# Kernel tuning notes

Measured on AMD Instinct MI355X. Metric: run time of the kernel, lower is better.

The kernel has to match this reference:

```python
import jax, jax.numpy as jnp
import numpy as np

THRESHOLD = 1.0
BETA = 0.9  # initial mem is zeros, so mem = beta*0 + u = u


def spike(u):
    # forward of SurrogateGradient: (u > threshold).float()
    return (u > THRESHOLD).astype(u.dtype)


def rope_tables(seq_len, head_dim, base=10000.0):
    inv_freq = 1.0 / (base ** (jnp.arange(0, head_dim, 2, dtype=jnp.float32) / head_dim))
    t = jnp.arange(seq_len, dtype=jnp.float32)
    freqs = jnp.einsum('i,j->ij', t, inv_freq)          # [S, d/2]
    emb = jnp.concatenate([freqs, freqs], axis=-1)       # [S, d]
    return jnp.cos(emb), jnp.sin(emb)


def apply_rope(x, cos, sin):
    # x: [B, S, H, d]
    x1, x2 = jnp.split(x, 2, axis=-1)
    rot = jnp.concatenate([-x2, x1], axis=-1)
    return x * cos[None, :, None, :] + rot * sin[None, :, None, :]


def setup_inputs() -> dict:
    key = jax.random.key(0)
    ks = jax.random.split(key, 5)
    B, S, D = 1, 2048, 2048
    std = 1.0 / np.sqrt(D)
    return {
        'x':  jax.random.normal(ks[0], (B, S, D), jnp.float32),
        'Wq': jax.random.normal(ks[1], (D, D), jnp.float32) * std,
        'Wk': jax.random.normal(ks[2], (D, D), jnp.float32) * std,
        'Wv': jax.random.normal(ks[3], (D, D), jnp.float32) * std,
        'Wo': jax.random.normal(ks[4], (D, D), jnp.float32) * std,
    }


def reference(x, Wq, Wk, Wv, Wo):
    B, S, D = x.shape
    H, hd = 16, 128
    scale = hd ** -0.5

    q = (x @ Wq).reshape(B, S, H, hd)
    k = (x @ Wk).reshape(B, S, H, hd)
    v = (x @ Wv).reshape(B, S, H, hd)

    # LIF: mem starts at zero -> mem = q; spike = (mem > threshold)
    sq, sk, sv = spike(q), spike(k), spike(v)

    cos, sin = rope_tables(S, hd)
    rq = apply_rope(sq, cos, sin)
    rk = apply_rope(sk, cos, sin)

    scores = jnp.einsum('bqhd,bkhd->bhqk', rq, rk) * scale  # [B,H,S,S]
    causal = jnp.tril(jnp.ones((S, S), dtype=bool))
    scores = jnp.where(causal[None, None], scores, -jnp.inf)
    attn = jax.nn.softmax(scores, axis=-1)

    out = jnp.einsum('bhqk,bkhd->bqhd', attn, sv).reshape(B, S, H * hd)
    return out @ Wo
```

## Files before the change

### kernel.cpp

```cpp
#include <hip/hip_runtime.h>

typedef unsigned short u16;
typedef unsigned int u32;
typedef u16 u16x4 __attribute__((ext_vector_type(4)));
typedef u16 u16x8 __attribute__((ext_vector_type(8)));
typedef float f32x4 __attribute__((ext_vector_type(4)));
typedef __bf16 bf16x8 __attribute__((ext_vector_type(8)));
typedef _Float16 f16x4 __attribute__((ext_vector_type(4)));
typedef _Float16 f16x8 __attribute__((ext_vector_type(8)));

#define DD 2048
#define SCALE_ATTN 0.08838834764831845f
#define DELTA 0.005f

#define GL16(g, l)                                                              \
  __builtin_amdgcn_global_load_lds((const __attribute__((address_space(1))) u32*)(g), \
                                   (__attribute__((address_space(3))) u32*)(l), 16, 0, 0)

__device__ __forceinline__ u16 f2bf(float f) {
  u32 u = __float_as_uint(f);
  u32 r = (u + 0x7FFFu + ((u >> 16) & 1u)) >> 16;
  return (u16)r;
}
__device__ __forceinline__ float bf2f(u16 h) { return __uint_as_float(((u32)h) << 16); }


__global__ void k_rope_tables(float* __restrict__ cosT, float* __restrict__ sinT) {
  int i = blockIdx.x * 256 + threadIdx.x;
  int s = i >> 6, j = i & 63;
  float e = (float)(2 * j) / 128.0f;
  float inv = 1.0f / powf(10000.0f, e);
  float fr = (float)s * inv;
  cosT[i] = cosf(fr);
  sinT[i] = sinf(fr);
}

__global__ void k_cvt_x(const float* __restrict__ x, _Float16* __restrict__ xf) {
  int i = (blockIdx.x * 256 + threadIdx.x) * 4;
  float4 v = *(const float4*)&x[i];
  f16x4 o = {(_Float16)v.x, (_Float16)v.y, (_Float16)v.z, (_Float16)v.w};
  *(f16x4*)&xf[i] = o;
}

__global__ void k_transpose_w(const float* __restrict__ Wq, const float* __restrict__ Wk,
                              const float* __restrict__ Wv, _Float16* __restrict__ Wq16,
                              _Float16* __restrict__ Wk16, _Float16* __restrict__ Wv16,
                              float* __restrict__ Wq32, float* __restrict__ Wk32,
                              float* __restrict__ Wv32) {
  const float* W = blockIdx.y == 0 ? Wq : (blockIdx.y == 1 ? Wk : Wv);
  _Float16* WT16 = blockIdx.y == 0 ? Wq16 : (blockIdx.y == 1 ? Wk16 : Wv16);
  float* WT32 = blockIdx.y == 0 ? Wq32 : (blockIdx.y == 1 ? Wk32 : Wv32);
  __shared__ float tile[32][33];
  int bk = blockIdx.x & 63, bn = blockIdx.x >> 6;
  int c = threadIdx.x & 31, r0 = threadIdx.x >> 5;
#pragma unroll
  for (int i = 0; i < 4; ++i) {
    int r = r0 + i * 8;
    tile[r][c] = W[(size_t)(bk * 32 + r) * DD + bn * 32 + c];
  }
  __syncthreads();
#pragma unroll
  for (int i = 0; i < 4; ++i) {
    int r = r0 + i * 8;
    float v = tile[c][r];
    size_t o = (size_t)(bn * 32 + r) * DD + bk * 32 + c;
    WT16[o] = (_Float16)v;
    WT32[o] = v;
  }
}

__global__ void k_transpose_bo(const float* __restrict__ W, u16* __restrict__ WhT) {
  __shared__ float tile[32][33];
  int bk = blockIdx.x & 63, bn = blockIdx.x >> 6;
  int c = threadIdx.x & 31, r0 = threadIdx.x >> 5;
#pragma unroll
  for (int i = 0; i < 4; ++i) {
    int r = r0 + i * 8;
    tile[r][c] = W[(size_t)(bk * 32 + r) * DD + bn * 32 + c];
  }
  __syncthreads();
#pragma unroll
  for (int i = 0; i < 4; ++i) {
    int r = r0 + i * 8;
    WhT[(size_t)(bn * 32 + r) * DD + bk * 32 + c] = f2bf(tile[c][r]);
  }
}

__global__ void k_transpose_bf16(const u16* __restrict__ in, u16* __restrict__ out) {
  __shared__ u16 tile[32][33];
  int bk = blockIdx.x & 63, bn = blockIdx.x >> 6;
  int c = threadIdx.x & 31, r0 = threadIdx.x >> 5;
#pragma unroll
  for (int i = 0; i < 4; ++i) {
    int r = r0 + i * 8;
    tile[r][c] = in[(size_t)(bk * 32 + r) * DD + bn * 32 + c];
  }
  __syncthreads();
#pragma unroll
  for (int i = 0; i < 4; ++i) {
    int r = r0 + i * 8;
    out[(size_t)(bn * 32 + r) * DD + bk * 32 + c] = tile[c][r];
  }
}

__global__ void k_rope_apply(u16* sq, u16* sk, const float* __restrict__ cosT,
                             const float* __restrict__ sinT) {
  int i = blockIdx.x * 256 + threadIdx.x;
  int s = i >> 10;
  int rest = i & 1023;
  int h = rest >> 6, j = rest & 63;
  size_t base = (size_t)s * DD + h * 128 + j;
  float c = cosT[(s << 6) | j], sn = sinT[(s << 6) | j];
  float a = bf2f(sq[base]), b = bf2f(sq[base + 64]);
  sq[base] = f2bf(a * c - b * sn);
  sq[base + 64] = f2bf(b * c + a * sn);
  a = bf2f(sk[base]);
  b = bf2f(sk[base + 64]);
  sk[base] = f2bf(a * c - b * sn);
  sk[base + 64] = f2bf(b * c + a * sn);
}

__global__ __launch_bounds__(256) void k_gemm_qkv(
    const _Float16* __restrict__ xf, const _Float16* __restrict__ BqT,
    const _Float16* __restrict__ BkT, const _Float16* __restrict__ BvT, u16* __restrict__ Sq,
    u16* __restrict__ Sk, u16* __restrict__ Sv, unsigned char* __restrict__ flagT) {
  __shared__ u16 lA[2 * 4096];
  __shared__ u16 lB[2 * 4096];

  const _Float16* BT = blockIdx.y == 0 ? BqT : (blockIdx.y == 1 ? BkT : BvT);
  u16* Out = blockIdx.y == 0 ? Sq : (blockIdx.y == 1 ? Sk : Sv);
  unsigned char* flT = flagT + (size_t)blockIdx.y * 4194304;

  int bid = blockIdx.x;
  int swz = (bid & 7) * 32 + (bid >> 3);
  int m0 = (swz >> 4) * 128, n0 = (swz & 15) * 128;

  int tid = threadIdx.x;
  int lane = tid & 63;
  int w = tid >> 6;
  int wr = (w >> 1) * 64, wc = (w & 1) * 64;
  int l15 = lane & 15, g8 = (lane >> 4) * 8;

  int ar0 = tid >> 2, ac0 = (tid & 3) << 3;
  int ar1 = (tid + 256) >> 2, ac1 = (tid & 3) << 3;

  f32x4 zero = {0.f, 0.f, 0.f, 0.f};
  f32x4 acc[4][4];
#pragma unroll
  for (int i = 0; i < 4; ++i)
#pragma unroll
    for (int j = 0; j < 4; ++j) acc[i][j] = zero;

  u16* laBase0 = lA + w * 512;
  u16* laBase1 = lA + 2048 + w * 512;
  u16* lbBase0 = lB + w * 512;
  u16* lbBase1 = lB + 2048 + w * 512;

  auto stage = [&](int buf, int vs) {
    int k0 = vs << 5;
    int bo = buf * 4096;
    GL16(&xf[(size_t)(m0 + ar0) * DD + k0 + ac0], laBase0 + bo);
    GL16(&xf[(size_t)(m0 + ar1) * DD + k0 + ac1], laBase1 + bo);
    GL16(&BT[(size_t)(n0 + ar0) * DD + k0 + ac0], lbBase0 + bo);
    GL16(&BT[(size_t)(n0 + ar1) * DD + k0 + ac1], lbBase1 + bo);
  };

  stage(0, 0);
  __syncthreads();
  for (int vs = 0; vs < 64; ++vs) {
    int cur = vs & 1;
    if (vs + 1 < 64) stage(cur ^ 1, vs + 1);
    const u16* la = lA + cur * 4096;
    const u16* lb = lB + cur * 4096;
    f16x8 af[4], bfr[4];
#pragma unroll
    for (int i = 0; i < 4; ++i) af[i] = *(const f16x8*)&la[(wr + i * 16 + l15) * 32 + g8];
#pragma unroll
    for (int j = 0; j < 4; ++j) bfr[j] = *(const f16x8*)&lb[(wc + j * 16 + l15) * 32 + g8];
#pragma unroll
    for (int i = 0; i < 4; ++i)
#pragma unroll
      for (int j = 0; j < 4; ++j)
        acc[i][j] = __builtin_amdgcn_mfma_f32_16x16x32_f16(af[i], bfr[j], acc[i][j], 0, 0, 0);
    __syncthreads();
  }

  int g4 = (lane >> 4) * 4;
#pragma unroll
  for (int i = 0; i < 4; ++i) {
    int row0 = m0 + wr + i * 16 + g4;
#pragma unroll
    for (int j = 0; j < 4; ++j) {
      int col = n0 + wc + j * 16 + l15;
      u32 fw = 0;
#pragma unroll
      for (int r = 0; r < 4; ++r) {
        float u = acc[i][j][r];
        Out[(size_t)(row0 + r) * DD + col] = (u > 1.0f) ? (u16)0x3F80 : (u16)0;
        if (fabsf(u - 1.0f) < DELTA) fw |= (1u << (8 * r));
      }
      *(u32*)&flT[(size_t)col * 2048 + row0] = fw;
    }
  }
}

__global__ __launch_bounds__(256) void k_compact(const unsigned char* __restrict__ flagT,
                                                 u32* __restrict__ cnt, u32* __restrict__ wlist) {
  __shared__ u32 wsum[4];
  int tid = threadIdx.x;
  int lane = tid & 63;
  int w = tid >> 6;
  size_t blockBase = (size_t)blockIdx.x * 16384;
  const u32* fp = (const u32*)(flagT + blockBase);
  unsigned long long fm = 0;
#pragma unroll
  for (int it = 0; it < 4; ++it) {
    u32 m16 = 0;
#pragma unroll
    for (int wd = 0; wd < 4; ++wd) {
      u32 v = fp[it * 1024 + tid * 4 + wd];
      m16 |= (((v >> 0) & 1u) | ((v >> 7) & 2u) | ((v >> 14) & 4u) | ((v >> 21) & 8u)) << (wd * 4);
    }
    fm |= (unsigned long long)m16 << (it * 16);
  }
  u32 c = (u32)__popcll(fm);
  u32 pre = c;
#pragma unroll
  for (int d = 1; d < 64; d <<= 1) {
    u32 t = __shfl_up(pre, d, 64);
    if (lane >= d) pre += t;
  }
  if (lane == 63) wsum[w] = pre;
  __syncthreads();
  u32 wbase = 0;
#pragma unroll
  for (int i = 0; i < 4; ++i)
    if (i < w) wbase += wsum[i];
  if (tid == 0) {
    u32 tot = wsum[0] + wsum[1] + wsum[2] + wsum[3];
    cnt[blockIdx.x] = tot > 256u ? 256u : tot;
  }
  u32 pos = wbase + pre - c;
  u32 outbase = (u32)blockIdx.x * 256u;
  while (fm) {
    int p = __ffsll((long long)fm) - 1;
    fm &= fm - 1;
    u32 e = (u32)blockBase + (u32)(p >> 4) * 4096u + (u32)tid * 16u + (u32)(p & 15);
    if (pos < 256u) wlist[outbase + pos] = e;
    ++pos;
  }
}

__global__ __launch_bounds__(256) void k_fixup(
    const float* __restrict__ x, const float* __restrict__ WqT, const float* __restrict__ WkT,
    const float* __restrict__ WvT, const u32* __restrict__ cnt, const u32* __restrict__ wlist,
    u16* __restrict__ Sq, u16* __restrict__ Sk, u16* __restrict__ Sv) {
  u32 wid = (blockIdx.x * 256 + threadIdx.x) >> 6;
  int lane = threadIdx.x & 63;
  for (u32 s = wid; s < 768u * 256u; s += 8192u) {
    u32 b = s % 768u, k = s / 768u;
    if (k >= cnt[b]) continue;
    u32 e = wlist[b * 256u + k];
    int i = (int)(e & 2047u);
    int j = (int)((e >> 11) & 2047u);
    int mat = (int)(e >> 22);
    const float* WT = mat == 0 ? WqT : (mat == 1 ? WkT : WvT);
    const float* xr = x + (size_t)i * DD;
    const float* wrw = WT + (size_t)j * DD;
    float u = 0.f;
#pragma unroll
    for (int t = 0; t < 8; ++t) {
      float4 a = *(const float4*)&xr[t * 256 + lane * 4];
      float4 bv = *(const float4*)&wrw[t * 256 + lane * 4];
      u = fmaf(a.x, bv.x, u);
      u = fmaf(a.y, bv.y, u);
      u = fmaf(a.z, bv.z, u);
      u = fmaf(a.w, bv.w, u);
    }
#pragma unroll
    for (int sh = 32; sh; sh >>= 1) u += __shfl_xor(u, sh);
    if (lane == 0) {
      u16* Out2 = mat == 0 ? Sq : (mat == 1 ? Sk : Sv);
      Out2[(size_t)i * DD + j] = (u > 1.0f) ? (u16)0x3F80 : (u16)0;
    }
  }
}

__global__ __launch_bounds__(256) void k_gemm_out(const u16* __restrict__ A,
                                                  const u16* __restrict__ BT,
                                                  float* __restrict__ C) {
  __shared__ u16 lA[2 * 4096];
  __shared__ u16 lB[2 * 4096];
  int bid = blockIdx.x;
  int swz = (bid & 7) * 32 + (bid >> 3);
  int m0 = (swz >> 4) * 128, n0 = (swz & 15) * 128;
  int tid = threadIdx.x;
  int lane = tid & 63;
  int w = tid >> 6;
  int wr = (w >> 1) * 64, wc = (w & 1) * 64;
  int l15 = lane & 15, g8 = (lane >> 4) * 8;
  int ar0 = tid >> 2, ac0 = (tid & 3) << 3;
  int ar1 = (tid + 256) >> 2, ac1 = (tid & 3) << 3;
  f32x4 zero = {0.f, 0.f, 0.f, 0.f};
  f32x4 acc[4][4];
#pragma unroll
  for (int i = 0; i < 4; ++i)
#pragma unroll
    for (int j = 0; j < 4; ++j) acc[i][j] = zero;

  u16* laBase0 = lA + w * 512;
  u16* laBase1 = lA + 2048 + w * 512;
  u16* lbBase0 = lB + w * 512;
  u16* lbBase1 = lB + 2048 + w * 512;

  auto stage = [&](int buf, int vs) {
    int k0 = vs << 5;
    int bo = buf * 4096;
    GL16(&A[(size_t)(m0 + ar0) * DD + k0 + ac0], laBase0 + bo);
    GL16(&A[(size_t)(m0 + ar1) * DD + k0 + ac1], laBase1 + bo);
    GL16(&BT[(size_t)(n0 + ar0) * DD + k0 + ac0], lbBase0 + bo);
    GL16(&BT[(size_t)(n0 + ar1) * DD + k0 + ac1], lbBase1 + bo);
  };

  stage(0, 0);
  __syncthreads();
  for (int vs = 0; vs < 64; ++vs) {
    int cur = vs & 1;
    if (vs + 1 < 64) stage(cur ^ 1, vs + 1);
    const u16* la = lA + cur * 4096;
    const u16* lb = lB + cur * 4096;
    bf16x8 af[4], bfr[4];
#pragma unroll
    for (int i = 0; i < 4; ++i) af[i] = *(const bf16x8*)&la[(wr + i * 16 + l15) * 32 + g8];
#pragma unroll
    for (int j = 0; j < 4; ++j) bfr[j] = *(const bf16x8*)&lb[(wc + j * 16 + l15) * 32 + g8];
#pragma unroll
    for (int i = 0; i < 4; ++i)
#pragma unroll
      for (int j = 0; j < 4; ++j)
        acc[i][j] = __builtin_amdgcn_mfma_f32_16x16x32_bf16(af[i], bfr[j], acc[i][j], 0, 0, 0);
    __syncthreads();
  }

  int g4 = (lane >> 4) * 4;
#pragma unroll
  for (int i = 0; i < 4; ++i) {
    int row0 = m0 + wr + i * 16 + g4;
#pragma unroll
    for (int j = 0; j < 4; ++j) {
      int col = n0 + wc + j * 16 + l15;
#pragma unroll
      for (int r = 0; r < 4; ++r) C[(size_t)(row0 + r) * DD + col] = acc[i][j][r];
    }
  }
}

__global__ __launch_bounds__(512) void k_attn(const u16* __restrict__ rq,
                                              const u16* __restrict__ rk,
                                              const u16* __restrict__ svT,
                                              u16* __restrict__ outp) {
  __shared__ u16 lrk[64 * 136];
  __shared__ u16 lsv[128 * 72];
  __shared__ u16 lP[8 * 16 * 72];

  int bid = blockIdx.x;
  int h = bid & 15;
  int i0 = bid >> 4;
  int qb = (i0 & 1) ? (15 - (i0 >> 1)) : (i0 >> 1);
  int q0 = qb * 128;

  int tid = threadIdx.x;
  int lane = tid & 63;
  int w = tid >> 6;
  int l15 = lane & 15;
  int g = lane >> 4;
  int qw = q0 + w * 16;
  int qpos = qw + l15;
  int pb = w * 1152 + l15 * 72;

  bf16x8 rqf[4];
#pragma unroll
  for (int ks = 0; ks < 4; ++ks)
    rqf[ks] = *(const bf16x8*)&rq[(size_t)qpos * DD + h * 128 + ks * 32 + g * 8];

  f32x4 zero = {0.f, 0.f, 0.f, 0.f};
  f32x4 acc[8];
#pragma unroll
  for (int dt = 0; dt < 8; ++dt) acc[dt] = zero;
  float mrun = -1e30f, lrun = 0.f;

  int nt = (q0 >> 6) + 2;
  for (int t = 0; t < nt; ++t) {
    int kv0 = t << 6;
    int r = tid >> 4, c8 = (tid & 15) << 3;
    u16x8 s0 = *(const u16x8*)&rk[(size_t)(kv0 + r) * DD + h * 128 + c8];
    int idx1 = tid + 512;
    int rB = idx1 >> 4, c8B = (idx1 & 15) << 3;
    u16x8 s2 = *(const u16x8*)&rk[(size_t)(kv0 + rB) * DD + h * 128 + c8B];
    int r2 = tid >> 3, d8 = (tid & 7) << 3;
    u16x8 s1 = *(const u16x8*)&svT[(size_t)(h * 128 + r2) * DD + kv0 + d8];
    int r2B = idx1 >> 3, d8B = (idx1 & 7) << 3;
    u16x8 s3 = *(const u16x8*)&svT[(size_t)(h * 128 + r2B) * DD + kv0 + d8B];

    __syncthreads();
    *(u16x8*)&lrk[r * 136 + c8] = s0;
    *(u16x8*)&lrk[rB * 136 + c8B] = s2;
    *(u16x8*)&lsv[r2 * 72 + d8] = s1;
    *(u16x8*)&lsv[r2B * 72 + d8B] = s3;
    __syncthreads();

    bool active = (kv0 <= qw + 15);
    if (active) {
      f32x4 sacc[4];
#pragma unroll
      for (int kt = 0; kt < 4; ++kt) sacc[kt] = zero;
#pragma unroll
      for (int kt = 0; kt < 4; ++kt)
#pragma unroll
        for (int ks = 0; ks < 4; ++ks) {
          bf16x8 a = *(const bf16x8*)&lrk[(kt * 16 + l15) * 136 + ks * 32 + g * 8];
          sacc[kt] = __builtin_amdgcn_mfma_f32_16x16x32_bf16(a, rqf[ks], sacc[kt], 0, 0, 0);
        }
      float p[4][4];
      float mx = -1e30f;
#pragma unroll
      for (int kt = 0; kt < 4; ++kt)
#pragma unroll
        for (int rr = 0; rr < 4; ++rr) {
          int kvpos = kv0 + kt * 16 + g * 4 + rr;
          float sc = sacc[kt][rr] * SCALE_ATTN;
          sc = (kvpos <= qpos) ? sc : -1e30f;
          p[kt][rr] = sc;
          mx = fmaxf(mx, sc);
        }
      mx = fmaxf(mx, __shfl_xor(mx, 16));
      mx = fmaxf(mx, __shfl_xor(mx, 32));
      float mnew = fmaxf(mrun, mx);
      float alpha = __expf(mrun - mnew);
      float rs = 0.f;
#pragma unroll
      for (int kt = 0; kt < 4; ++kt)
#pragma unroll
        for (int rr = 0; rr < 4; ++rr) {
          float e = __expf(p[kt][rr] - mnew);
          p[kt][rr] = e;
          rs += e;
        }
      rs += __shfl_xor(rs, 16);
      rs += __shfl_xor(rs, 32);
      lrun = lrun * alpha + rs;
      mrun = mnew;
      float al[4];
#pragma unroll
      for (int rr = 0; rr < 4; ++rr) al[rr] = __shfl(alpha, (lane & 48) | (g * 4 + rr), 64);
#pragma unroll
      for (int dt = 0; dt < 8; ++dt)
#pragma unroll
        for (int rr = 0; rr < 4; ++rr) acc[dt][rr] *= al[rr];
#pragma unroll
      for (int kt = 0; kt < 4; ++kt) {
        u16x4 pk = {f2bf(p[kt][0]), f2bf(p[kt][1]), f2bf(p[kt][2]), f2bf(p[kt][3])};
        *(u16x4*)&lP[pb + kt * 16 + g * 4] = pk;
      }
    }
    __syncthreads();
    if (active) {
      bf16x8 pa0 = *(const bf16x8*)&lP[pb + g * 8];
      bf16x8 pa1 = *(const bf16x8*)&lP[pb + 32 + g * 8];
#pragma unroll
      for (int dt = 0; dt < 8; ++dt) {
        bf16x8 b0 = *(const bf16x8*)&lsv[(dt * 16 + l15) * 72 + g * 8];
        acc[dt] = __builtin_amdgcn_mfma_f32_16x16x32_bf16(pa0, b0, acc[dt], 0, 0, 0);
        bf16x8 b1 = *(const bf16x8*)&lsv[(dt * 16 + l15) * 72 + 32 + g * 8];
        acc[dt] = __builtin_amdgcn_mfma_f32_16x16x32_bf16(pa1, b1, acc[dt], 0, 0, 0);
      }
    }
  }

  float linv[4];
#pragma unroll
  for (int rr = 0; rr < 4; ++rr)
    linv[rr] = 1.0f / __shfl(lrun, (lane & 48) | (g * 4 + rr), 64);
#pragma unroll
  for (int dt = 0; dt < 8; ++dt)
#pragma unroll
    for (int rr = 0; rr < 4; ++rr) {
      int row = qw + g * 4 + rr;
      outp[(size_t)row * DD + h * 128 + dt * 16 + l15] = f2bf(acc[dt][rr] * linv[rr]);
    }
}

extern "C" void kernel_launch(void* const* d_in, const int* in_sizes, int n_in, void* d_out,
                              int out_size, void* d_ws, size_t ws_size, hipStream_t stream) {
  (void)in_sizes;
  (void)n_in;
  (void)out_size;
  const float* x = (const float*)d_in[0];
  const float* Wq = (const float*)d_in[1];
  const float* Wk = (const float*)d_in[2];
  const float* Wv = (const float*)d_in[3];
  const float* Wo = (const float*)d_in[4];
  float* out = (float*)d_out;

  const size_t SZ = (size_t)DD * DD;
  size_t need = 35 * SZ + 2 * (size_t)2048 * 64 * 4;
  if (ws_size < need) return;

  char* p = (char*)d_ws;
  auto a2 = [&](void) {
    void* q = (void*)p;
    p += SZ * 2;
    return q;
  };
  _Float16* xf = (_Float16*)a2();
  _Float16* WqT16 = (_Float16*)a2();
  _Float16* WkT16 = (_Float16*)a2();
  _Float16* WvT16 = (_Float16*)a2();
  u16* BoT = (u16*)a2();
  u16* sq = (u16*)a2();
  u16* sk = (u16*)a2();
  u16* sv = (u16*)a2();
  u16* svT = (u16*)a2();
  u16* outp = (u16*)a2();
  float* WqT32 = (float*)p;
  p += SZ * 4;
  float* WkT32 = (float*)p;
  p += SZ * 4;
  float* WvT32 = (float*)p;
  p += SZ * 4;
  unsigned char* flagT = (unsigned char*)p;
  p += 3 * SZ;
  float* cosT = (float*)p;
  p += (size_t)2048 * 64 * 4;
  float* sinT = (float*)p;
  u32* cnt = (u32*)svT;
  u32* wlist = cnt + 1024;

  k_rope_tables<<<512, 256, 0, stream>>>(cosT, sinT);
  k_cvt_x<<<4096, 256, 0, stream>>>(x, xf);
  k_transpose_w<<<dim3(4096, 3, 1), 256, 0, stream>>>(Wq, Wk, Wv, WqT16, WkT16, WvT16, WqT32,
                                                      WkT32, WvT32);
  k_transpose_bo<<<4096, 256, 0, stream>>>(Wo, BoT);
  k_gemm_qkv<<<dim3(256, 3, 1), 256, 0, stream>>>(xf, WqT16, WkT16, WvT16, sq, sk, sv, flagT);
  k_compact<<<768, 256, 0, stream>>>(flagT, cnt, wlist);
  k_fixup<<<2048, 256, 0, stream>>>(x, WqT32, WkT32, WvT32, cnt, wlist, sq, sk, sv);
  k_rope_apply<<<8192, 256, 0, stream>>>(sq, sk, cosT, sinT);
  k_transpose_bf16<<<4096, 256, 0, stream>>>(sv, svT);
  k_attn<<<256, 512, 0, stream>>>(sq, sk, svT, outp);
  k_gemm_out<<<256, 256, 0, stream>>>(outp, BoT, out);
}
```

Measured before the change: 320.0 us.

## Shrink attention query tile to 64 rows with 256-thread blocks

The attention kernel now uses 64-query blocks of 4 waves instead of 128-query blocks of 8 waves, which doubles the grid to 512 blocks. Blocks are issued in descending query-block order, longest first. Because the 64-row query tile lines up with the 64-wide KV tile, the per-wave causal activity check is gone, and so is the barrier between the P write and the P read, since each wave reads only its own P slice. In exchange, every block loads the K/V tiles for half as many queries, which doubles the global-to-LDS traffic per query.

```diff
diff --git a/kernel.cpp b/kernel.cpp
--- a/kernel.cpp
+++ b/kernel.cpp
@@ -355,19 +355,19 @@
   }
 }
 
-__global__ __launch_bounds__(512) void k_attn(const u16* __restrict__ rq,
+__global__ __launch_bounds__(256) void k_attn(const u16* __restrict__ rq,
                                               const u16* __restrict__ rk,
                                               const u16* __restrict__ svT,
                                               u16* __restrict__ outp) {
   __shared__ u16 lrk[64 * 136];
   __shared__ u16 lsv[128 * 72];
-  __shared__ u16 lP[8 * 16 * 72];
+  __shared__ u16 lP[4 * 16 * 72];
 
   int bid = blockIdx.x;
   int h = bid & 15;
   int i0 = bid >> 4;
-  int qb = (i0 & 1) ? (15 - (i0 >> 1)) : (i0 >> 1);
-  int q0 = qb * 128;
+  int qb = 31 - i0;
+  int q0 = qb * 64;
 
   int tid = threadIdx.x;
   int lane = tid & 63;
@@ -389,91 +389,88 @@
   for (int dt = 0; dt < 8; ++dt) acc[dt] = zero;
   float mrun = -1e30f, lrun = 0.f;
 
-  int nt = (q0 >> 6) + 2;
+  int nt = (q0 >> 6) + 1;
   for (int t = 0; t < nt; ++t) {
     int kv0 = t << 6;
-    int r = tid >> 4, c8 = (tid & 15) << 3;
-    u16x8 s0 = *(const u16x8*)&rk[(size_t)(kv0 + r) * DD + h * 128 + c8];
-    int idx1 = tid + 512;
-    int rB = idx1 >> 4, c8B = (idx1 & 15) << 3;
-    u16x8 s2 = *(const u16x8*)&rk[(size_t)(kv0 + rB) * DD + h * 128 + c8B];
-    int r2 = tid >> 3, d8 = (tid & 7) << 3;
-    u16x8 s1 = *(const u16x8*)&svT[(size_t)(h * 128 + r2) * DD + kv0 + d8];
-    int r2B = idx1 >> 3, d8B = (idx1 & 7) << 3;
-    u16x8 s3 = *(const u16x8*)&svT[(size_t)(h * 128 + r2B) * DD + kv0 + d8B];
-
+    u16x8 sk_[4], sv_[4];
+#pragma unroll
+    for (int p = 0; p < 4; ++p) {
+      int idx = tid + p * 256;
+      int r = idx >> 4, c8 = (idx & 15) << 3;
+      sk_[p] = *(const u16x8*)&rk[(size_t)(kv0 + r) * DD + h * 128 + c8];
+      int r2 = idx >> 3, d8 = (idx & 7) << 3;
+      sv_[p] = *(const u16x8*)&svT[(size_t)(h * 128 + r2) * DD + kv0 + d8];
+    }
     __syncthreads();
-    *(u16x8*)&lrk[r * 136 + c8] = s0;
-    *(u16x8*)&lrk[rB * 136 + c8B] = s2;
-    *(u16x8*)&lsv[r2 * 72 + d8] = s1;
-    *(u16x8*)&lsv[r2B * 72 + d8B] = s3;
+#pragma unroll
+    for (int p = 0; p < 4; ++p) {
+      int idx = tid + p * 256;
+      int r = idx >> 4, c8 = (idx & 15) << 3;
+      *(u16x8*)&lrk[r * 136 + c8] = sk_[p];
+      int r2 = idx >> 3, d8 = (idx & 7) << 3;
+      *(u16x8*)&lsv[r2 * 72 + d8] = sv_[p];
+    }
     __syncthreads();
 
-    bool active = (kv0 <= qw + 15);
-    if (active) {
-      f32x4 sacc[4];
-#pragma unroll
-      for (int kt = 0; kt < 4; ++kt) sacc[kt] = zero;
-#pragma unroll
-      for (int kt = 0; kt < 4; ++kt)
-#pragma unroll
-        for (int ks = 0; ks < 4; ++ks) {
-          bf16x8 a = *(const bf16x8*)&lrk[(kt * 16 + l15) * 136 + ks * 32 + g * 8];
-          sacc[kt] = __builtin_amdgcn_mfma_f32_16x16x32_bf16(a, rqf[ks], sacc[kt], 0, 0, 0);
-        }
-      float p[4][4];
-      float mx = -1e30f;
-#pragma unroll
-      for (int kt = 0; kt < 4; ++kt)
-#pragma unroll
-        for (int rr = 0; rr < 4; ++rr) {
-          int kvpos = kv0 + kt * 16 + g * 4 + rr;
-          float sc = sacc[kt][rr] * SCALE_ATTN;
-          sc = (kvpos <= qpos) ? sc : -1e30f;
-          p[kt][rr] = sc;
-          mx = fmaxf(mx, sc);
-        }
-      mx = fmaxf(mx, __shfl_xor(mx, 16));
-      mx = fmaxf(mx, __shfl_xor(mx, 32));
-      float mnew = fmaxf(mrun, mx);
-      float alpha = __expf(mrun - mnew);
-      float rs = 0.f;
-#pragma unroll
-      for (int kt = 0; kt < 4; ++kt)
-#pragma unroll
-        for (int rr = 0; rr < 4; ++rr) {
-          float e = __expf(p[kt][rr] - mnew);
-          p[kt][rr] = e;
-          rs += e;
-        }
-      rs += __shfl_xor(rs, 16);
-      rs += __shfl_xor(rs, 32);
-      lrun = lrun * alpha + rs;
-      mrun = mnew;
-      float al[4];
-#pragma unroll
-      for (int rr = 0; rr < 4; ++rr) al[rr] = __shfl(alpha, (lane & 48) | (g * 4 + rr), 64);
-#pragma unroll
-      for (int dt = 0; dt < 8; ++dt)
-#pragma unroll
-        for (int rr = 0; rr < 4; ++rr) acc[dt][rr] *= al[rr];
-#pragma unroll
-      for (int kt = 0; kt < 4; ++kt) {
-        u16x4 pk = {f2bf(p[kt][0]), f2bf(p[kt][1]), f2bf(p[kt][2]), f2bf(p[kt][3])};
-        *(u16x4*)&lP[pb + kt * 16 + g * 4] = pk;
+    f32x4 sacc[4];
+#pragma unroll
+    for (int kt = 0; kt < 4; ++kt) sacc[kt] = zero;
+#pragma unroll
+    for (int kt = 0; kt < 4; ++kt)
+#pragma unroll
+      for (int ks = 0; ks < 4; ++ks) {
+        bf16x8 a = *(const bf16x8*)&lrk[(kt * 16 + l15) * 136 + ks * 32 + g * 8];
+        sacc[kt] = __builtin_amdgcn_mfma_f32_16x16x32_bf16(a, rqf[ks], sacc[kt], 0, 0, 0);
       }
-    }
-    __syncthreads();
-    if (active) {
-      bf16x8 pa0 = *(const bf16x8*)&lP[pb + g * 8];
-      bf16x8 pa1 = *(const bf16x8*)&lP[pb + 32 + g * 8];
-#pragma unroll
-      for (int dt = 0; dt < 8; ++dt) {
-        bf16x8 b0 = *(const bf16x8*)&lsv[(dt * 16 + l15) * 72 + g * 8];
-        acc[dt] = __builtin_amdgcn_mfma_f32_16x16x32_bf16(pa0, b0, acc[dt], 0, 0, 0);
-        bf16x8 b1 = *(const bf16x8*)&lsv[(dt * 16 + l15) * 72 + 32 + g * 8];
-        acc[dt] = __builtin_amdgcn_mfma_f32_16x16x32_bf16(pa1, b1, acc[dt], 0, 0, 0);
+    float p[4][4];
+    float mx = -1e30f;
+#pragma unroll
+    for (int kt = 0; kt < 4; ++kt)
+#pragma unroll
+      for (int rr = 0; rr < 4; ++rr) {
+        int kvpos = kv0 + kt * 16 + g * 4 + rr;
+        float sc = sacc[kt][rr] * SCALE_ATTN;
+        sc = (kvpos <= qpos) ? sc : -1e30f;
+        p[kt][rr] = sc;
+        mx = fmaxf(mx, sc);
       }
+    mx = fmaxf(mx, __shfl_xor(mx, 16));
+    mx = fmaxf(mx, __shfl_xor(mx, 32));
+    float mnew = fmaxf(mrun, mx);
+    float alpha = __expf(mrun - mnew);
+    float rs = 0.f;
+#pragma unroll
+    for (int kt = 0; kt < 4; ++kt)
+#pragma unroll
+      for (int rr = 0; rr < 4; ++rr) {
+        float e = __expf(p[kt][rr] - mnew);
+        p[kt][rr] = e;
+        rs += e;
+      }
+    rs += __shfl_xor(rs, 16);
+    rs += __shfl_xor(rs, 32);
+    lrun = lrun * alpha + rs;
+    mrun = mnew;
+    float al[4];
+#pragma unroll
+    for (int rr = 0; rr < 4; ++rr) al[rr] = __shfl(alpha, (lane & 48) | (g * 4 + rr), 64);
+#pragma unroll
+    for (int dt = 0; dt < 8; ++dt)
+#pragma unroll
+      for (int rr = 0; rr < 4; ++rr) acc[dt][rr] *= al[rr];
+#pragma unroll
+    for (int kt = 0; kt < 4; ++kt) {
+      u16x4 pk = {f2bf(p[kt][0]), f2bf(p[kt][1]), f2bf(p[kt][2]), f2bf(p[kt][3])};
+      *(u16x4*)&lP[pb + kt * 16 + g * 4] = pk;
+    }
+    bf16x8 pa0 = *(const bf16x8*)&lP[pb + g * 8];
+    bf16x8 pa1 = *(const bf16x8*)&lP[pb + 32 + g * 8];
+#pragma unroll
+    for (int dt = 0; dt < 8; ++dt) {
+      bf16x8 b0 = *(const bf16x8*)&lsv[(dt * 16 + l15) * 72 + g * 8];
+      acc[dt] = __builtin_amdgcn_mfma_f32_16x16x32_bf16(pa0, b0, acc[dt], 0, 0, 0);
+      bf16x8 b1 = *(const bf16x8*)&lsv[(dt * 16 + l15) * 72 + 32 + g * 8];
+      acc[dt] = __builtin_amdgcn_mfma_f32_16x16x32_bf16(pa1, b1, acc[dt], 0, 0, 0);
     }
   }
 
@@ -546,6 +543,6 @@
   k_fixup<<<2048, 256, 0, stream>>>(x, WqT32, WkT32, WvT32, cnt, wlist, sq, sk, sv);
   k_rope_apply<<<8192, 256, 0, stream>>>(sq, sk, cosT, sinT);
   k_transpose_bf16<<<4096, 256, 0, stream>>>(sv, svT);
-  k_attn<<<256, 512, 0, stream>>>(sq, sk, svT, outp);
+  k_attn<<<512, 256, 0, stream>>>(sq, sk, svT, outp);
   k_gemm_out<<<256, 256, 0, stream>>>(outp, BoT, out);
 }
```

New measurement: 307.1 us. 4.0% less time.
